# Performance work log

Measured on AMD Instinct MI355X. Metric: run time of the kernel, lower is better.

## Reference

```python
import jax, jax.numpy as jnp
import numpy as np

B, H, W, C_IN, C_HID = 32, 64, 64, 384, 128

def setup_inputs() -> dict:
    key = jax.random.key(0)
    k0, k1, k2 = jax.random.split(key, 3)
    dino_features = jax.random.normal(k0, (B, H, W, C_IN), dtype=jnp.float32)
    # Xavier-uniform(gain=0.5) bounds for conv weights, HWIO layout
    fan1 = C_IN * 9 + C_HID * 9
    lim1 = 0.5 * np.sqrt(6.0 / fan1)
    W1 = jax.random.uniform(k1, (3, 3, C_IN, C_HID), minval=-lim1, maxval=lim1, dtype=jnp.float32)
    b1 = jnp.zeros((C_HID,), dtype=jnp.float32)
    fan2 = C_HID + 1
    lim2 = 0.5 * np.sqrt(6.0 / fan2)
    W2 = jax.random.uniform(k2, (1, 1, C_HID, 1), minval=-lim2, maxval=lim2, dtype=jnp.float32)
    b2 = jnp.zeros((1,), dtype=jnp.float32)
    return {"dino_features": dino_features, "W1": W1, "b1": b1, "W2": W2, "b2": b2}

def _conv(x, w, pad):
    # x: NHWC, w: HWIO -> NHWC
    return jax.lax.conv_general_dilated(
        x, w, window_strides=(1, 1), padding=pad,
        dimension_numbers=("NHWC", "HWIO", "NHWC"))

def reference(dino_features, W1, b1, W2, b2):
    # conv3x3 (pad 1) -> ReLU -> conv1x1 -> sigmoid; output (B,H,W,1)
    h = jax.nn.relu(_conv(dino_features, W1, ((1, 1), (1, 1))) + b1)
    logits = _conv(h, W2, ((0, 0), (0, 0))) + b2
    return jax.nn.sigmoid(logits)
```

## Files before the change

kernel.cpp:

```cpp
#include <hip/hip_runtime.h>
#include <hip/hip_bf16.h>
#include <math.h>


typedef __attribute__((ext_vector_type(8))) unsigned short ushort8;
typedef __attribute__((ext_vector_type(8))) __bf16 bf16x8;
typedef __attribute__((ext_vector_type(4))) float floatx4;

static __device__ __forceinline__ unsigned short f2bf_rne(float f) {
  union { float f; unsigned int u; } x; x.f = f;
  unsigned int u = x.u;
  return (unsigned short)((u + 0x7fffu + ((u >> 16) & 1u)) >> 16);
}

static __device__ __forceinline__ ushort8 pack8(const float* v) {
  ushort8 r;
#pragma unroll
  for (int i = 0; i < 4; ++i) {
    __hip_bfloat162 p = __float22bfloat162_rn(make_float2(v[2 * i], v[2 * i + 1]));
    union { __hip_bfloat162 b; unsigned int u; } c;
    c.b = p;
    r[2 * i] = (unsigned short)(c.u & 0xffffu);
    r[2 * i + 1] = (unsigned short)(c.u >> 16);
  }
  return r;
}

__global__ void prep_w1_kernel(const float* __restrict__ W1,
                               unsigned short* __restrict__ W1b) {
  __shared__ unsigned short tile[32 * 128];
  const int kk = blockIdx.x;
  const int o = kk / 12;
  const int chunk = kk - o * 12;
  const float* src = W1 + (o * 384 + chunk * 32) * 128;
  const int t = threadIdx.x;
#pragma unroll
  for (int i = 0; i < 16; ++i) {
    int idx = t + i * 256;
    int c = idx >> 7;
    int n = idx & 127;
    tile[n * 32 + c] = f2bf_rne(src[idx]);
  }
  __syncthreads();
  unsigned short* dst = W1b + kk * 4096;
#pragma unroll
  for (int i = 0; i < 16; ++i) {
    int idx = t + i * 256;
    dst[idx] = tile[idx];
  }
}

__global__ __launch_bounds__(256) void conv_fused_kernel(
    const float* __restrict__ x, const unsigned short* __restrict__ W1b,
    const float* __restrict__ b1, const float* __restrict__ W2,
    const float* __restrict__ b2, float* __restrict__ out) {
  __shared__ alignas(16) unsigned short Ah[2 * 4320];
  __shared__ float hsum[64 * 4];

  const int t = threadIdx.x;
  const int w = t >> 6;
  const int lane = t & 63;
  const int g = lane >> 4;
  const int lr = lane & 15;

  const int img = blockIdx.x >> 6;
  const int tileId = blockIdx.x & 63;
  const int ty0 = (tileId >> 2) << 2;
  const int tx0 = (tileId & 3) << 4;

  int svalid[2];
  int soff[2];
  int sloff[2];
  const bool act1 = t < 176;
#pragma unroll
  for (int j = 0; j < 2; ++j) {
    int i = t + j * 256;
    int px = i >> 2, sub = i & 3;
    int hy = (px * 57) >> 10;
    int hx = px - hy * 18;
    int iy = ty0 + hy - 1, ix = tx0 + hx - 1;
    int v = ((unsigned)iy < 64u) && ((unsigned)ix < 64u);
    if (j == 1 && !act1) v = 0;
    svalid[j] = v;
    int iyc = v ? iy : 0, ixc = v ? ix : 0;
    soff[j] = ((((img << 6) + iyc) << 6) + ixc) * 384 + sub * 8;
    sloff[j] = px * 40 + sub * 8;
  }

  const int boff = ((w * 32 + lr) << 5) + (g << 3);
  const int aoffl = lr * 40 + (g << 3);

  floatx4 acc[4][2] = {};

  const float b1v0 = b1[w * 32 + lr];
  const float b1v1 = b1[w * 32 + 16 + lr];
  const float w2v0 = W2[w * 32 + lr];
  const float w2v1 = W2[w * 32 + 16 + lr];

  float sreg[2][8];
#pragma unroll
  for (int j = 0; j < 2; ++j)
#pragma unroll
    for (int e = 0; e < 8; ++e) sreg[j][e] = 0.0f;

#pragma unroll
  for (int j = 0; j < 2; ++j) {
    if (svalid[j]) {
      *(float4*)&sreg[j][0] = *(const float4*)(x + soff[j]);
      *(float4*)&sreg[j][4] = *(const float4*)(x + soff[j] + 4);
    }
  }
  *(ushort8*)&Ah[sloff[0]] = pack8(sreg[0]);
  if (act1) *(ushort8*)&Ah[sloff[1]] = pack8(sreg[1]);
#pragma unroll
  for (int j = 0; j < 2; ++j) {
    if (svalid[j]) {
      *(float4*)&sreg[j][0] = *(const float4*)(x + soff[j] + 32);
      *(float4*)&sreg[j][4] = *(const float4*)(x + soff[j] + 36);
    }
  }
  __syncthreads();

  for (int c = 0; c < 12; ++c) {
    const int rb = (c & 1) * 4320;
    const int wb = 4320 - rb;

    if (c < 11) {
      *(ushort8*)&Ah[wb + sloff[0]] = pack8(sreg[0]);
      if (act1) *(ushort8*)&Ah[wb + sloff[1]] = pack8(sreg[1]);
    }

#pragma unroll
    for (int ox = 0; ox < 3; ++ox) {
      bf16x8 bf[3][2];
#pragma unroll
      for (int oy = 0; oy < 3; ++oy) {
        const unsigned short* bp =
            W1b + ((((oy * 3 + ox) * 12 + c) << 12)) + boff;
        bf[oy][0] = *(const bf16x8*)bp;
        bf[oy][1] = *(const bf16x8*)(bp + 512);
      }
      if (ox == 2 && c < 10) {
        const int off = (c + 2) << 5;
#pragma unroll
        for (int j = 0; j < 2; ++j) {
          if (svalid[j]) {
            *(float4*)&sreg[j][0] = *(const float4*)(x + soff[j] + off);
            *(float4*)&sreg[j][4] = *(const float4*)(x + soff[j] + off + 4);
          }
        }
      }
#pragma unroll
      for (int h = 0; h < 6; ++h) {
        const bf16x8 af = *(const bf16x8*)&Ah[rb + h * 720 + ox * 40 + aoffl];
#pragma unroll
        for (int oy = 0; oy < 3; ++oy) {
          const int mi = h - oy;
          if (mi >= 0 && mi < 4) {
            acc[mi][0] = __builtin_amdgcn_mfma_f32_16x16x32_bf16(
                af, bf[oy][0], acc[mi][0], 0, 0, 0);
            acc[mi][1] = __builtin_amdgcn_mfma_f32_16x16x32_bf16(
                af, bf[oy][1], acc[mi][1], 0, 0, 0);
          }
        }
      }
    }
    __syncthreads();
  }

#pragma unroll
  for (int mi = 0; mi < 4; ++mi) {
#pragma unroll
    for (int r = 0; r < 4; ++r) {
      float h0 = fmaxf(acc[mi][0][r] + b1v0, 0.0f);
      float h1 = fmaxf(acc[mi][1][r] + b1v1, 0.0f);
      float v = h0 * w2v0 + h1 * w2v1;
      v += __shfl_xor(v, 1);
      v += __shfl_xor(v, 2);
      v += __shfl_xor(v, 4);
      v += __shfl_xor(v, 8);
      if (lr == 0) {
        int m = mi * 16 + g * 4 + r;
        hsum[m * 4 + w] = v;
      }
    }
  }
  __syncthreads();
  if (t < 64) {
    float s = hsum[t * 4 + 0] + hsum[t * 4 + 1] + hsum[t * 4 + 2] +
              hsum[t * 4 + 3] + b2[0];
    float sig = 1.0f / (1.0f + expf(-s));
    int prow = t >> 4, pcol = t & 15;
    out[((((img << 6) + ty0 + prow) << 6) + tx0 + pcol)] = sig;
  }
}

extern "C" void kernel_launch(void* const* d_in, const int* in_sizes, int n_in,
                              void* d_out, int out_size, void* d_ws, size_t ws_size,
                              hipStream_t stream) {
  const float* x  = (const float*)d_in[0];
  const float* W1 = (const float*)d_in[1];
  const float* b1 = (const float*)d_in[2];
  const float* W2 = (const float*)d_in[3];
  const float* b2 = (const float*)d_in[4];
  float* out = (float*)d_out;
  unsigned short* W1b = (unsigned short*)d_ws;

  prep_w1_kernel<<<108, 256, 0, stream>>>(W1, W1b);
  conv_fused_kernel<<<2048, 256, 0, stream>>>(x, W1b, b1, W2, b2, out);
}
```

Measured before the change: 374.1 us.

## Double-buffer weight fragments across taps and repack LDS tile without padding

```diff
diff --git a/kernel.cpp b/kernel.cpp
--- a/kernel.cpp
+++ b/kernel.cpp
@@ -50,11 +50,11 @@
   }
 }
 
-__global__ __launch_bounds__(256) void conv_fused_kernel(
+__global__ __launch_bounds__(256, 2) void conv_fused_kernel(
     const float* __restrict__ x, const unsigned short* __restrict__ W1b,
     const float* __restrict__ b1, const float* __restrict__ W2,
     const float* __restrict__ b2, float* __restrict__ out) {
-  __shared__ alignas(16) unsigned short Ah[2 * 4320];
+  __shared__ alignas(16) unsigned short Ah[2 * 3456];
   __shared__ float hsum[64 * 4];
 
   const int t = threadIdx.x;
@@ -84,11 +84,11 @@
     svalid[j] = v;
     int iyc = v ? iy : 0, ixc = v ? ix : 0;
     soff[j] = ((((img << 6) + iyc) << 6) + ixc) * 384 + sub * 8;
-    sloff[j] = px * 40 + sub * 8;
+    sloff[j] = (sub * 108 + px) << 3;
   }
 
   const int boff = ((w * 32 + lr) << 5) + (g << 3);
-  const int aoffl = lr * 40 + (g << 3);
+  const int aoffl = (g * 108 + lr) << 3;
 
   floatx4 acc[4][2] = {};
 
@@ -119,11 +119,20 @@
       *(float4*)&sreg[j][4] = *(const float4*)(x + soff[j] + 36);
     }
   }
+
+  bf16x8 bf[2][3][2];
+#pragma unroll
+  for (int oy = 0; oy < 3; ++oy) {
+    const unsigned short* bp = W1b + ((oy * 3 + 0) * 12 << 12) + boff;
+    bf[0][oy][0] = *(const bf16x8*)bp;
+    bf[0][oy][1] = *(const bf16x8*)(bp + 512);
+  }
   __syncthreads();
 
+#pragma unroll
   for (int c = 0; c < 12; ++c) {
-    const int rb = (c & 1) * 4320;
-    const int wb = 4320 - rb;
+    const int rb = (c & 1) * 3456;
+    const int wb = 3456 - rb;
 
     if (c < 11) {
       *(ushort8*)&Ah[wb + sloff[0]] = pack8(sreg[0]);
@@ -132,35 +141,48 @@
 
 #pragma unroll
     for (int ox = 0; ox < 3; ++ox) {
-      bf16x8 bf[3][2];
-#pragma unroll
-      for (int oy = 0; oy < 3; ++oy) {
-        const unsigned short* bp =
-            W1b + ((((oy * 3 + ox) * 12 + c) << 12)) + boff;
-        bf[oy][0] = *(const bf16x8*)bp;
-        bf[oy][1] = *(const bf16x8*)(bp + 512);
+      const int p = (c + ox) & 1;
+      if (ox < 2) {
+#pragma unroll
+        for (int oy = 0; oy < 3; ++oy) {
+          const unsigned short* bp =
+              W1b + ((((oy * 3 + ox + 1) * 12 + c) << 12)) + boff;
+          bf[1 - p][oy][0] = *(const bf16x8*)bp;
+          bf[1 - p][oy][1] = *(const bf16x8*)(bp + 512);
+        }
+      } else {
+        if (c < 10) {
+          const int off = (c + 2) << 5;
+#pragma unroll
+          for (int j = 0; j < 2; ++j) {
+            if (svalid[j]) {
+              *(float4*)&sreg[j][0] = *(const float4*)(x + soff[j] + off);
+              *(float4*)&sreg[j][4] = *(const float4*)(x + soff[j] + off + 4);
+            }
+          }
+        }
+        if (c < 11) {
+#pragma unroll
+          for (int oy = 0; oy < 3; ++oy) {
+            const unsigned short* bp =
+                W1b + ((((oy * 3 + 0) * 12 + (c + 1)) << 12)) + boff;
+            bf[1 - p][oy][0] = *(const bf16x8*)bp;
+            bf[1 - p][oy][1] = *(const bf16x8*)(bp + 512);
+          }
+        }
       }
-      if (ox == 2 && c < 10) {
-        const int off = (c + 2) << 5;
-#pragma unroll
-        for (int j = 0; j < 2; ++j) {
-          if (svalid[j]) {
-            *(float4*)&sreg[j][0] = *(const float4*)(x + soff[j] + off);
-            *(float4*)&sreg[j][4] = *(const float4*)(x + soff[j] + off + 4);
-          }
-        }
-      }
 #pragma unroll
       for (int h = 0; h < 6; ++h) {
-        const bf16x8 af = *(const bf16x8*)&Ah[rb + h * 720 + ox * 40 + aoffl];
+        const bf16x8 af =
+            *(const bf16x8*)&Ah[rb + ((h * 18 + ox) << 3) + aoffl];
 #pragma unroll
         for (int oy = 0; oy < 3; ++oy) {
           const int mi = h - oy;
           if (mi >= 0 && mi < 4) {
             acc[mi][0] = __builtin_amdgcn_mfma_f32_16x16x32_bf16(
-                af, bf[oy][0], acc[mi][0], 0, 0, 0);
+                af, bf[p][oy][0], acc[mi][0], 0, 0, 0);
             acc[mi][1] = __builtin_amdgcn_mfma_f32_16x16x32_bf16(
-                af, bf[oy][1], acc[mi][1], 0, 0, 0);
+                af, bf[p][oy][1], acc[mi][1], 0, 0, 0);
           }
         }
       }
```

After: 373.1 us. About the same (-0.3%).
